# Kernel tuning notes

Hardware: AMD Instinct MI355X
Metric: run time of the kernel (lower is better)

Reference implementation:

```python
import jax, jax.numpy as jnp
import numpy as np
from jax import lax

B, C_IN, N, C_OUT, K = 16, 128, 2048, 256, 20
EPS = 1e-5


def setup_inputs() -> dict:
    key = jax.random.key(0)
    k1, k2 = jax.random.split(key)
    x = jax.random.normal(k1, (B, C_IN, N), dtype=jnp.float32)
    W = jax.random.normal(k2, (C_OUT, 2 * C_IN), dtype=jnp.float32) * (1.0 / np.sqrt(2 * C_IN))
    gamma = jnp.ones((C_OUT,), dtype=jnp.float32)
    beta = jnp.zeros((C_OUT,), dtype=jnp.float32)
    return {"x": x, "W": W, "gamma": gamma, "beta": beta, "k": K}


def _knn_inds(x, k):
    # squared pairwise distance: (B, N, N); computed with no grad (stop_gradient)
    xs = lax.stop_gradient(x)
    inner = jnp.einsum('bcn,bcm->bnm', xs, xs)
    sq = jnp.sum(xs * xs, axis=1)  # (B, N)
    pd = sq[:, :, None] - 2.0 * inner + sq[:, None, :]
    _, inds = lax.top_k(-pd, k)  # smallest distances -> (B, N, k)
    return inds


def reference(x, W, gamma, beta, k):
    knn = _knn_inds(x, k)                                   # (B, N, k) int
    # gather neighbours: neigh[b,c,n,j] = x[b,c,knn[b,n,j]]
    neigh = jax.vmap(lambda xb, kb: xb[:, kb])(x, knn)      # (B, C, N, k)
    central = jnp.broadcast_to(x[:, :, :, None], neigh.shape)
    edge = jnp.concatenate([central, neigh - central], axis=1)  # (B, 2C, N, k)
    # 1x1 conv (bias-free) as GEMM
    y = jnp.einsum('oc,bcnk->bonk', W, edge)                # (B, C_out, N, k)
    # BatchNorm2d (training-mode batch stats) + affine
    mean = jnp.mean(y, axis=(0, 2, 3), keepdims=True)
    var = jnp.var(y, axis=(0, 2, 3), keepdims=True)
    y = (y - mean) * lax.rsqrt(var + EPS)
    y = y * gamma[None, :, None, None] + beta[None, :, None, None]
    y = jax.nn.relu(y)
    return jnp.max(y, axis=3)                               # (B, C_out, N)
```

## Files before the change

### kernel.cpp

```cpp
#include <hip/hip_runtime.h>

#define B_   16
#define CIN  128
#define NPT  2048
#define COUT 256
#define KNN  20
#define KEEP 16
#define SIFT 32
#define EPS  1e-5f
#define DBIAS 256.0f

#define SQ_OFF   0ull
#define IDX_OFF  131072ull
#define UT_OFF   2752512ull
#define VT_OFF   36306944ull
#define GS_OFF   69861376ull
#define ST_OFF   69865472ull
#define AMAX_OFF 69871616ull
#define AMIN_OFF 103426048ull
#define WS_NEED_FUSED 136980480ull
#define XT_OFF   UT_OFF
#define XHT_OFF  VT_OFF

typedef _Float16 f16x8 __attribute__((ext_vector_type(8)));
typedef float    f32x4 __attribute__((ext_vector_type(4)));
typedef float    f32x2 __attribute__((ext_vector_type(2)));

__global__ __launch_bounds__(256) void prep_kernel(const float* __restrict__ x,
                                                   float* __restrict__ xT,
                                                   _Float16* __restrict__ xhT,
                                                   float* __restrict__ sqh) {
    __shared__ float Ls[128 * 68];
    __shared__ float ps[4 * 64];
    const int id  = blockIdx.x;
    const int xcd = id & 7, qq = id >> 3;
    const int b   = xcd + ((qq >> 5) << 3);
    const int n0  = (qq & 31) * 64;
    const int t = threadIdx.x;
    const float* xb = x + (size_t)b * CIN * NPT;
    #pragma unroll
    for (int e = 0; e < 8; ++e) {
        int f = e * 256 + t;
        int c = f >> 4, n4 = (f & 15) << 2;
        *(float4*)&Ls[c * 68 + n4] = *(const float4*)&xb[(size_t)c * NPT + n0 + n4];
    }
    __syncthreads();
    {
        int nl = t & 63, part = t >> 6;
        float acc = 0.f;
        #pragma unroll
        for (int j = 0; j < 32; ++j) {
            float vh = (float)(_Float16)Ls[(part * 32 + j) * 68 + nl];
            acc += vh * vh;
        }
        ps[part * 64 + nl] = acc;
    }
    #pragma unroll
    for (int e = 0; e < 2; ++e) {
        int u = e * 256 + t;
        int nl = u >> 3, ck = (u & 7) << 4;
        float vv[16];
        #pragma unroll
        for (int j = 0; j < 16; ++j) vv[j] = Ls[(ck + j) * 68 + nl];
        size_t row = (size_t)b * NPT + n0 + nl;
        #pragma unroll
        for (int j = 0; j < 4; ++j) {
            float4 w = {vv[4 * j], vv[4 * j + 1], vv[4 * j + 2], vv[4 * j + 3]};
            *(float4*)&xT[row * CIN + ck + 4 * j] = w;
        }
        f16x8 h0, h1;
        #pragma unroll
        for (int j = 0; j < 8; ++j) { h0[j] = (_Float16)vv[j]; h1[j] = (_Float16)vv[8 + j]; }
        *(f16x8*)&xhT[row * CIN + ck] = h0;
        *(f16x8*)&xhT[row * CIN + ck + 8] = h1;
    }
    __syncthreads();
    if (t < 64) sqh[b * NPT + n0 + t] = ps[t] + ps[64 + t] + ps[128 + t] + ps[192 + t];
}

__global__ void wconv_kernel(const float* __restrict__ W,
                             _Float16* __restrict__ Wu,
                             _Float16* __restrict__ Wv) {
    int gid = blockIdx.x * 256 + threadIdx.x;
    int o = gid >> 7, c = gid & 127;
    float w1 = W[o * 256 + c], w2 = W[o * 256 + 128 + c];
    Wu[gid] = (_Float16)(w1 - w2);
    Wv[gid] = (_Float16)w2;
}

__device__ __forceinline__ void stage_pts(const _Float16* __restrict__ xhb,
                                          _Float16* buf, int base_n, int t) {
    const int l15 = t & 15, ks = t >> 6;
    const int quad = (t >> 4) & 3;
    const int c = ks * 32 + quad * 8;
    #pragma unroll
    for (int e = 0; e < 4; ++e) {
        const int n = base_n + e * 16 + l15;
        const _Float16* src = xhb + (size_t)n * CIN + c;
        _Float16* dst = buf + (size_t)(e * 256 + (t & 192)) * 8;
        __builtin_amdgcn_global_load_lds(
            (const __attribute__((address_space(1))) void*)src,
            (__attribute__((address_space(3))) void*)dst, 16, 0, 0);
    }
}

__device__ __forceinline__ void stage_tile16(const _Float16* __restrict__ srcl,
                                             _Float16* dsthalf) {
    #pragma unroll
    for (int e = 0; e < 4; ++e) {
        __builtin_amdgcn_global_load_lds(
            (const __attribute__((address_space(1))) void*)(srcl + e * 32),
            (__attribute__((address_space(3))) void*)(dsthalf + (size_t)e * 512),
            16, 0, 0);
    }
}

__global__ __launch_bounds__(256, 2) void knn_kernel(const _Float16* __restrict__ xhT,
                                                     const float* __restrict__ sqh,
                                                     int* __restrict__ surv_out) {
    __shared__ char smraw[59392];
    _Float16* bufA = (_Float16*)smraw;
    float*    sqm  = (float*)(smraw + 18432);

    const int id  = blockIdx.x;
    const int xcd = id & 7, qq = id >> 3;
    const int b   = xcd + ((qq >> 5) << 3);
    const int q0  = (qq & 31) * 64;
    const int t  = threadIdx.x;
    const int lane = t & 63, wv = t >> 6;
    const int l15 = lane & 15, quad = lane >> 4;
    const _Float16* xhb = xhT + (size_t)b * NPT * CIN;

    #pragma unroll
    for (int e = 0; e < 8; ++e)
        sqm[e * 256 + t] = sqh[b * NPT + e * 256 + t] + DBIAS;

    stage_pts(xhb, bufA, q0, t);
    __syncthreads();

    f16x8 af[4][4];
    #pragma unroll
    for (int qh = 0; qh < 4; ++qh)
        #pragma unroll
        for (int ks = 0; ks < 4; ++ks)
            af[qh][ks] = *(const f16x8*)(bufA + (size_t)((qh * 4 + ks) * 64 + lane) * 8);
    __syncthreads();

    _Float16* wbuf = (_Float16*)(smraw + 26624 + wv * 8192);
    float*    DtW  = (float*)(smraw + wv * 4608);
    const _Float16* srcl = xhb + (size_t)(wv * 16 + l15) * CIN + quad * 8;

    stage_tile16(srcl, wbuf);

    float bd[KEEP];
    #pragma unroll
    for (int i = 0; i < KEEP; ++i) bd[i] = 3.0e38f;

    #pragma unroll 1
    for (int ss = 0; ss < 32; ++ss) {
        const int mb = ss * 64 + wv * 16;
        asm volatile("s_waitcnt vmcnt(0)" ::: "memory");
        __builtin_amdgcn_sched_barrier(0);
        const _Float16* cur = wbuf + (ss & 1) * 2048;
        f16x8 bf[4];
        #pragma unroll
        for (int ks = 0; ks < 4; ++ks)
            bf[ks] = *(const f16x8*)(cur + ks * 512 + lane * 8);
        float sm_ = sqm[mb + l15];
        asm volatile("s_waitcnt lgkmcnt(0)" ::: "memory");
        __builtin_amdgcn_sched_barrier(0);
        if (ss < 31)
            stage_tile16(srcl + (size_t)(ss + 1) * 64 * CIN,
                         wbuf + ((ss + 1) & 1) * 2048);
        __builtin_amdgcn_sched_barrier(0);
        f32x4 acc[4];
        #pragma unroll
        for (int qh = 0; qh < 4; ++qh) acc[qh] = (f32x4){0.f, 0.f, 0.f, 0.f};
        #pragma unroll
        for (int ks = 0; ks < 4; ++ks)
            #pragma unroll
            for (int qh = 0; qh < 4; ++qh)
                acc[qh] = __builtin_amdgcn_mfma_f32_16x16x32_f16(af[qh][ks], bf[ks], acc[qh], 0, 0, 0);
        const unsigned om = (unsigned)(mb + l15);
        #pragma unroll
        for (int qh = 0; qh < 4; ++qh) {
            #pragma unroll
            for (int rg = 0; rg < 4; ++rg) {
                int q = qh * 16 + quad * 4 + rg;
                float d = sm_ - 2.f * acc[qh][rg];
                DtW[q * 18 + l15] = __uint_as_float((__float_as_uint(d) & 0xFFFFF800u) | om);
            }
        }
        float nk[16];
        {
            const float* myrow = DtW + lane * 18;
            #pragma unroll
            for (int p = 0; p < 8; ++p) {
                f32x2 v = *(const f32x2*)(myrow + 2 * p);
                nk[2 * p] = v[0]; nk[2 * p + 1] = v[1];
            }
        }
        #pragma unroll
        for (int kk = 2; kk <= 16; kk <<= 1) {
            #pragma unroll
            for (int j = kk >> 1; j > 0; j >>= 1) {
                #pragma unroll
                for (int i = 0; i < 16; ++i) {
                    int p = i ^ j;
                    if (p > i) {
                        float a = nk[i], c = nk[p];
                        float lo = fminf(a, c), hi = fmaxf(a, c);
                        if ((i & kk) == 0) { nk[i] = lo; nk[p] = hi; }
                        else               { nk[i] = hi; nk[p] = lo; }
                    }
                }
            }
        }
        #pragma unroll
        for (int i = 0; i < 16; ++i) bd[i] = fminf(bd[i], nk[15 - i]);
        #pragma unroll
        for (int j = 8; j > 0; j >>= 1) {
            #pragma unroll
            for (int i = 0; i < 16; ++i) {
                int p = i ^ j;
                if (p > i) {
                    float a = bd[i], c = bd[p];
                    bd[i] = fminf(a, c);
                    bd[p] = fmaxf(a, c);
                }
            }
        }
    }

    __syncthreads();

    float* Keys = (float*)smraw;
    #pragma unroll
    for (int i = 0; i < KEEP; ++i)
        Keys[lane * 65 + wv * KEEP + i] = bd[i];
    __syncthreads();
    {
        int cnt[KEEP];
        #pragma unroll
        for (int i = 0; i < KEEP; ++i) cnt[i] = 0;
        #pragma unroll 4
        for (int j = 0; j < 64; ++j) {
            float kj = Keys[lane * 65 + j];
            #pragma unroll
            for (int i = 0; i < KEEP; ++i)
                cnt[i] += (kj < bd[i]) ? 1 : 0;
        }
        int* dst = surv_out + ((size_t)b * NPT + q0 + lane) * SIFT;
        #pragma unroll
        for (int i = 0; i < KEEP; ++i)
            if (cnt[i] < SIFT)
                dst[cnt[i]] = (int)(__float_as_uint(bd[i]) & 0x7FFu);
    }
}

__global__ __launch_bounds__(256, 4) void refine_kernel(const float* __restrict__ xT,
                                                        const int* __restrict__ surv,
                                                        int* __restrict__ knn_out) {
    __shared__ float  Qs[16 * 128];
    __shared__ int    sidx[16 * 32];
    __shared__ double ddL[16 * 32];
    const int id  = blockIdx.x;
    const int xcd = id & 7, qq = id >> 3;
    const int b   = xcd + ((qq >> 7) << 3);
    const int q0  = (qq & 127) * 16;
    const int t = threadIdx.x;
    const float* xTb = xT + (size_t)b * NPT * CIN;
    #pragma unroll
    for (int e = 0; e < 2; ++e)
        sidx[e * 256 + t] = surv[((size_t)b * NPT + q0) * SIFT + e * 256 + t];
    #pragma unroll
    for (int e = 0; e < 2; ++e) {
        int f = e * 256 + t;
        int row = f >> 5, c4 = (f & 31) << 2;
        *(float4*)&Qs[row * 128 + c4] = *(const float4*)&xTb[(size_t)(q0 + row) * CIN + c4];
    }
    __syncthreads();
    const int g = t >> 3, j = t & 7;
    #pragma unroll 1
    for (int it = 0; it < 16; ++it) {
        int pair = it * 32 + g;
        int q = pair >> 5, k = pair & 31;
        int m = sidx[q * 32 + k];
        const float* mrow = xTb + (size_t)m * CIN + j * 16;
        const float* qrow = Qs + q * 128 + j * 16;
        float4 a0 = *(const float4*)&mrow[0];
        float4 a1 = *(const float4*)&mrow[4];
        float4 a2 = *(const float4*)&mrow[8];
        float4 a3 = *(const float4*)&mrow[12];
        float4 c0 = *(const float4*)&qrow[0];
        float4 c1 = *(const float4*)&qrow[4];
        float4 c2 = *(const float4*)&qrow[8];
        float4 c3 = *(const float4*)&qrow[12];
        double ss = 0.0, d0;
        d0 = (double)c0.x - (double)a0.x; ss = fma(d0, d0, ss);
        d0 = (double)c0.y - (double)a0.y; ss = fma(d0, d0, ss);
        d0 = (double)c0.z - (double)a0.z; ss = fma(d0, d0, ss);
        d0 = (double)c0.w - (double)a0.w; ss = fma(d0, d0, ss);
        d0 = (double)c1.x - (double)a1.x; ss = fma(d0, d0, ss);
        d0 = (double)c1.y - (double)a1.y; ss = fma(d0, d0, ss);
        d0 = (double)c1.z - (double)a1.z; ss = fma(d0, d0, ss);
        d0 = (double)c1.w - (double)a1.w; ss = fma(d0, d0, ss);
        d0 = (double)c2.x - (double)a2.x; ss = fma(d0, d0, ss);
        d0 = (double)c2.y - (double)a2.y; ss = fma(d0, d0, ss);
        d0 = (double)c2.z - (double)a2.z; ss = fma(d0, d0, ss);
        d0 = (double)c2.w - (double)a2.w; ss = fma(d0, d0, ss);
        d0 = (double)c3.x - (double)a3.x; ss = fma(d0, d0, ss);
        d0 = (double)c3.y - (double)a3.y; ss = fma(d0, d0, ss);
        d0 = (double)c3.z - (double)a3.z; ss = fma(d0, d0, ss);
        d0 = (double)c3.w - (double)a3.w; ss = fma(d0, d0, ss);
        ss += __shfl_xor(ss, 1, 8);
        ss += __shfl_xor(ss, 2, 8);
        ss += __shfl_xor(ss, 4, 8);
        if (j == 0) ddL[q * 32 + k] = ss;
    }
    __syncthreads();
    const int q = t >> 4, kk = (t & 15) << 1;
    int* dst = knn_out + ((size_t)b * NPT + q0 + q) * KNN;
    #pragma unroll
    for (int e = 0; e < 2; ++e) {
        int k = kk + e;
        double mine = ddL[q * 32 + k];
        int c = 0;
        #pragma unroll 4
        for (int jx = 0; jx < SIFT; ++jx)
            c += (ddL[q * 32 + jx] < mine) ? 1 : 0;
        if (c < KNN) dst[c] = sidx[q * 32 + k];
    }
}

__global__ __launch_bounds__(256, 2) void knn_kernel_fb(const _Float16* __restrict__ xhT,
                                                        const float* __restrict__ xT,
                                                        const float* __restrict__ sqh,
                                                        int* __restrict__ knn_out) {
    __shared__ char smraw[59392];
    _Float16* bufA = (_Float16*)smraw;
    float*    sqm  = (float*)(smraw + 18432);

    const int b  = blockIdx.y;
    const int q0 = blockIdx.x * 64;
    const int t  = threadIdx.x;
    const int lane = t & 63, wv = t >> 6;
    const int l15 = lane & 15, quad = lane >> 4;
    const _Float16* xhb = xhT + (size_t)b * NPT * CIN;

    #pragma unroll
    for (int e = 0; e < 8; ++e)
        sqm[e * 256 + t] = sqh[b * NPT + e * 256 + t] + DBIAS;

    stage_pts(xhb, bufA, q0, t);
    __syncthreads();

    f16x8 af[4][4];
    #pragma unroll
    for (int qh = 0; qh < 4; ++qh)
        #pragma unroll
        for (int ks = 0; ks < 4; ++ks)
            af[qh][ks] = *(const f16x8*)(bufA + (size_t)((qh * 4 + ks) * 64 + lane) * 8);
    __syncthreads();

    _Float16* wbuf = (_Float16*)(smraw + 26624 + wv * 8192);
    float*    DtW  = (float*)(smraw + wv * 4608);
    const _Float16* srcl = xhb + (size_t)(wv * 16 + l15) * CIN + quad * 8;
    stage_tile16(srcl, wbuf);

    float bd[KEEP];
    #pragma unroll
    for (int i = 0; i < KEEP; ++i) bd[i] = 3.0e38f;

    #pragma unroll 1
    for (int ss = 0; ss < 32; ++ss) {
        const int mb = ss * 64 + wv * 16;
        asm volatile("s_waitcnt vmcnt(0)" ::: "memory");
        __builtin_amdgcn_sched_barrier(0);
        const _Float16* cur = wbuf + (ss & 1) * 2048;
        f16x8 bf[4];
        #pragma unroll
        for (int ks = 0; ks < 4; ++ks)
            bf[ks] = *(const f16x8*)(cur + ks * 512 + lane * 8);
        float sm_ = sqm[mb + l15];
        asm volatile("s_waitcnt lgkmcnt(0)" ::: "memory");
        __builtin_amdgcn_sched_barrier(0);
        if (ss < 31)
            stage_tile16(srcl + (size_t)(ss + 1) * 64 * CIN,
                         wbuf + ((ss + 1) & 1) * 2048);
        __builtin_amdgcn_sched_barrier(0);
        f32x4 acc[4];
        #pragma unroll
        for (int qh = 0; qh < 4; ++qh) acc[qh] = (f32x4){0.f, 0.f, 0.f, 0.f};
        #pragma unroll
        for (int ks = 0; ks < 4; ++ks)
            #pragma unroll
            for (int qh = 0; qh < 4; ++qh)
                acc[qh] = __builtin_amdgcn_mfma_f32_16x16x32_f16(af[qh][ks], bf[ks], acc[qh], 0, 0, 0);
        const unsigned om = (unsigned)(mb + l15);
        #pragma unroll
        for (int qh = 0; qh < 4; ++qh) {
            #pragma unroll
            for (int rg = 0; rg < 4; ++rg) {
                int q = qh * 16 + quad * 4 + rg;
                float d = sm_ - 2.f * acc[qh][rg];
                DtW[q * 18 + l15] = __uint_as_float((__float_as_uint(d) & 0xFFFFF800u) | om);
            }
        }
        float nk[16];
        {
            const float* myrow = DtW + lane * 18;
            #pragma unroll
            for (int p = 0; p < 8; ++p) {
                f32x2 v = *(const f32x2*)(myrow + 2 * p);
                nk[2 * p] = v[0]; nk[2 * p + 1] = v[1];
            }
        }
        #pragma unroll
        for (int kk = 2; kk <= 16; kk <<= 1) {
            #pragma unroll
            for (int j = kk >> 1; j > 0; j >>= 1) {
                #pragma unroll
                for (int i = 0; i < 16; ++i) {
                    int p = i ^ j;
                    if (p > i) {
                        float a = nk[i], c = nk[p];
                        float lo = fminf(a, c), hi = fmaxf(a, c);
                        if ((i & kk) == 0) { nk[i] = lo; nk[p] = hi; }
                        else               { nk[i] = hi; nk[p] = lo; }
                    }
                }
            }
        }
        #pragma unroll
        for (int i = 0; i < 16; ++i) bd[i] = fminf(bd[i], nk[15 - i]);
        #pragma unroll
        for (int j = 8; j > 0; j >>= 1) {
            #pragma unroll
            for (int i = 0; i < 16; ++i) {
                int p = i ^ j;
                if (p > i) {
                    float a = bd[i], c = bd[p];
                    bd[i] = fminf(a, c);
                    bd[p] = fmaxf(a, c);
                }
            }
        }
    }

    __syncthreads();

    float*  Keys = (float*)smraw;
    int*    Surv = (int*)(smraw + 16640);
    double* ddL  = (double*)(smraw + 25088);
    #pragma unroll
    for (int i = 0; i < KEEP; ++i)
        Keys[lane * 65 + wv * KEEP + i] = bd[i];
    __syncthreads();
    {
        int cnt[KEEP];
        #pragma unroll
        for (int i = 0; i < KEEP; ++i) cnt[i] = 0;
        #pragma unroll 4
        for (int j = 0; j < 64; ++j) {
            float kj = Keys[lane * 65 + j];
            #pragma unroll
            for (int i = 0; i < KEEP; ++i)
                cnt[i] += (kj < bd[i]) ? 1 : 0;
        }
        __syncthreads();
        #pragma unroll
        for (int i = 0; i < KEEP; ++i)
            if (cnt[i] < SIFT)
                Surv[lane * 33 + cnt[i]] = (int)(__float_as_uint(bd[i]) & 0x7FFu);
    }
    __syncthreads();

    int ms[8];
    #pragma unroll
    for (int k = 0; k < 8; ++k) ms[k] = Surv[lane * 33 + wv * 8 + k] & 2047;
    double dd8[8];
    #pragma unroll
    for (int k = 0; k < 8; ++k) dd8[k] = 0.0;
    const float* xTb = xT + (size_t)b * NPT * CIN;
    const float* qrow = xTb + (size_t)(q0 + lane) * CIN;
    #pragma unroll 1
    for (int ch = 0; ch < 8; ++ch) {
        double qd[16];
        #pragma unroll
        for (int j = 0; j < 4; ++j) {
            float4 qv = *(const float4*)&qrow[ch * 16 + 4 * j];
            qd[4 * j] = (double)qv.x; qd[4 * j + 1] = (double)qv.y;
            qd[4 * j + 2] = (double)qv.z; qd[4 * j + 3] = (double)qv.w;
        }
        #pragma unroll
        for (int k = 0; k < 8; ++k) {
            const float* mrow = xTb + (size_t)ms[k] * CIN + ch * 16;
            float4 ma = *(const float4*)&mrow[0];
            float4 mb2 = *(const float4*)&mrow[4];
            float4 mc = *(const float4*)&mrow[8];
            float4 md = *(const float4*)&mrow[12];
            double ss = dd8[k], d0;
            d0 = qd[0]  - (double)ma.x;  ss = fma(d0, d0, ss);
            d0 = qd[1]  - (double)ma.y;  ss = fma(d0, d0, ss);
            d0 = qd[2]  - (double)ma.z;  ss = fma(d0, d0, ss);
            d0 = qd[3]  - (double)ma.w;  ss = fma(d0, d0, ss);
            d0 = qd[4]  - (double)mb2.x; ss = fma(d0, d0, ss);
            d0 = qd[5]  - (double)mb2.y; ss = fma(d0, d0, ss);
            d0 = qd[6]  - (double)mb2.z; ss = fma(d0, d0, ss);
            d0 = qd[7]  - (double)mb2.w; ss = fma(d0, d0, ss);
            d0 = qd[8]  - (double)mc.x;  ss = fma(d0, d0, ss);
            d0 = qd[9]  - (double)mc.y;  ss = fma(d0, d0, ss);
            d0 = qd[10] - (double)mc.z;  ss = fma(d0, d0, ss);
            d0 = qd[11] - (double)mc.w;  ss = fma(d0, d0, ss);
            d0 = qd[12] - (double)md.x;  ss = fma(d0, d0, ss);
            d0 = qd[13] - (double)md.y;  ss = fma(d0, d0, ss);
            d0 = qd[14] - (double)md.z;  ss = fma(d0, d0, ss);
            d0 = qd[15] - (double)md.w;  ss = fma(d0, d0, ss);
            dd8[k] = ss;
        }
    }
    #pragma unroll
    for (int k = 0; k < 8; ++k) ddL[lane * 33 + wv * 8 + k] = dd8[k];
    __syncthreads();
    int* dst = knn_out + ((size_t)b * NPT + q0 + lane) * KNN;
    #pragma unroll
    for (int k = 0; k < 8; ++k) {
        int c = 0;
        #pragma unroll 4
        for (int j = 0; j < SIFT; ++j)
            c += (ddL[lane * 33 + j] < dd8[k]) ? 1 : 0;
        if (c < KNN) dst[c] = ms[k];
    }
}

__global__ __launch_bounds__(256) void uv_gemm_h(const _Float16* __restrict__ xhT,
                                                 const _Float16* __restrict__ Wu,
                                                 const _Float16* __restrict__ Wv,
                                                 float* __restrict__ uT,
                                                 float* __restrict__ vT) {
    __shared__ _Float16 Bx[8192];
    const int id  = blockIdx.x;
    const int xcd = id & 7, qq = id >> 3;
    const int b   = xcd + ((qq >> 5) << 3);
    const int n0  = (qq & 31) * 64;
    const int t = threadIdx.x;
    const int lane = t & 63, w = t >> 6, l15 = lane & 15, quad = lane >> 4;
    stage_pts(xhT + (size_t)b * NPT * CIN, Bx, n0, t);
    __syncthreads();
    f16x8 bf[4];
    #pragma unroll
    for (int ks = 0; ks < 4; ++ks)
        bf[ks] = *(const f16x8*)(Bx + (size_t)((w * 4 + ks) * 64 + lane) * 8);
    const int n = n0 + w * 16 + l15;
    #pragma unroll 1
    for (int ot = 0; ot < 16; ++ot) {
        const _Float16* wu = Wu + (size_t)(ot * 16 + l15) * 128 + quad * 8;
        const _Float16* wv2 = Wv + (size_t)(ot * 16 + l15) * 128 + quad * 8;
        f32x4 au = (f32x4){0.f, 0.f, 0.f, 0.f};
        f32x4 av = (f32x4){0.f, 0.f, 0.f, 0.f};
        #pragma unroll
        for (int ks = 0; ks < 4; ++ks) {
            f16x8 a_u = *(const f16x8*)(wu + ks * 32);
            f16x8 a_v = *(const f16x8*)(wv2 + ks * 32);
            au = __builtin_amdgcn_mfma_f32_16x16x32_f16(a_u, bf[ks], au, 0, 0, 0);
            av = __builtin_amdgcn_mfma_f32_16x16x32_f16(a_v, bf[ks], av, 0, 0, 0);
        }
        size_t base = ((size_t)b * NPT + n) * COUT + ot * 16 + quad * 4;
        *(f32x4*)&uT[base] = au;
        *(f32x4*)&vT[base] = av;
    }
}

__global__ __launch_bounds__(256) void uv_gemm(const float* __restrict__ x,
                                               const float* __restrict__ W,
                                               float* __restrict__ uT,
                                               float* __restrict__ vT) {
    __shared__ float Ax[32 * 64];
    __shared__ float Bu[32 * 68];
    __shared__ float Bv[32 * 68];
    const int b  = blockIdx.z;
    const int n0 = blockIdx.x * 64;
    const int o0 = blockIdx.y * 64;
    const int t  = threadIdx.x;
    const int tx = t & 15, ty = t >> 4;
    const float* xb = x + (size_t)b * CIN * NPT;
    float au[4][4], av_[4][4];
    #pragma unroll
    for (int i = 0; i < 4; ++i)
        #pragma unroll
        for (int j = 0; j < 4; ++j) { au[i][j] = 0.f; av_[i][j] = 0.f; }
    #pragma unroll 1
    for (int kc = 0; kc < 4; ++kc) {
        const int c0 = kc * 32;
        __syncthreads();
        #pragma unroll
        for (int e = 0; e < 2; ++e) {
            int f = e * 256 + t;
            int cz = f >> 4, ni = (f & 15) << 2;
            *(float4*)&Ax[(cz << 6) + ni] = *(const float4*)&xb[(size_t)(c0 + cz) * NPT + n0 + ni];
        }
        #pragma unroll
        for (int e = 0; e < 8; ++e) {
            int ii = e * 256 + t;
            int cz = ii & 31, oj = ii >> 5;
            float w1 = W[(size_t)(o0 + oj) * 256 + c0 + cz];
            float w2 = W[(size_t)(o0 + oj) * 256 + 128 + c0 + cz];
            Bu[cz * 68 + oj] = w1 - w2;
            Bv[cz * 68 + oj] = w2;
        }
        __syncthreads();
        #pragma unroll 8
        for (int cz = 0; cz < 32; ++cz) {
            const float4 a4 = *(const float4*)&Ax[(cz << 6) + (tx << 2)];
            float bu0 = Bu[cz * 68 + (ty << 2) + 0], bv0 = Bv[cz * 68 + (ty << 2) + 0];
            float bu1 = Bu[cz * 68 + (ty << 2) + 1], bv1 = Bv[cz * 68 + (ty << 2) + 1];
            float bu2 = Bu[cz * 68 + (ty << 2) + 2], bv2 = Bv[cz * 68 + (ty << 2) + 2];
            float bu3 = Bu[cz * 68 + (ty << 2) + 3], bv3 = Bv[cz * 68 + (ty << 2) + 3];
            au[0][0] += a4.x * bu0; au[0][1] += a4.x * bu1; au[0][2] += a4.x * bu2; au[0][3] += a4.x * bu3;
            au[1][0] += a4.y * bu0; au[1][1] += a4.y * bu1; au[1][2] += a4.y * bu2; au[1][3] += a4.y * bu3;
            au[2][0] += a4.z * bu0; au[2][1] += a4.z * bu1; au[2][2] += a4.z * bu2; au[2][3] += a4.z * bu3;
            au[3][0] += a4.w * bu0; au[3][1] += a4.w * bu1; au[3][2] += a4.w * bu2; au[3][3] += a4.w * bu3;
            av_[0][0] += a4.x * bv0; av_[0][1] += a4.x * bv1; av_[0][2] += a4.x * bv2; av_[0][3] += a4.x * bv3;
            av_[1][0] += a4.y * bv0; av_[1][1] += a4.y * bv1; av_[1][2] += a4.y * bv2; av_[1][3] += a4.y * bv3;
            av_[2][0] += a4.z * bv0; av_[2][1] += a4.z * bv1; av_[2][2] += a4.z * bv2; av_[2][3] += a4.z * bv3;
            av_[3][0] += a4.w * bv0; av_[3][1] += a4.w * bv1; av_[3][2] += a4.w * bv2; av_[3][3] += a4.w * bv3;
        }
    }
    #pragma unroll
    for (int i = 0; i < 4; ++i) {
        int n = n0 + (tx << 2) + i;
        size_t base = ((size_t)b * NPT + n) * COUT + o0 + (ty << 2);
        float4 u4 = {au[i][0], au[i][1], au[i][2], au[i][3]};
        float4 v4 = {av_[i][0], av_[i][1], av_[i][2], av_[i][3]};
        *(float4*)&uT[base] = u4;
        *(float4*)&vT[base] = v4;
    }
}

__global__ __launch_bounds__(256) void gather_stats(const float* __restrict__ uT,
                                                    const float* __restrict__ vT,
                                                    const int* __restrict__ knn_in,
                                                    double* __restrict__ gsum,
                                                    float* __restrict__ aMax,
                                                    float* __restrict__ aMin) {
    __shared__ int sidx[16 * KNN];
    const int id  = blockIdx.x;
    const int xcd = id & 7, qq = id >> 3;
    const int b   = xcd + ((qq >> 7) << 3);
    const int inner = qq & 127;
    const int n0  = (inner >> 2) * 64 + (inner & 3) * 16;
    const int o   = threadIdx.x;
    for (int e = o; e < 16 * KNN; e += 256)
        sidx[e] = knn_in[((size_t)b * NPT + n0) * KNN + e];
    __syncthreads();
    const float* ub = uT + ((size_t)b * NPT + n0) * COUT + o;
    const float* vb = vT + (size_t)b * NPT * COUT + o;
    float* amx = aMax + ((size_t)b * NPT + n0) * COUT + o;
    float* amn = aMin + ((size_t)b * NPT + n0) * COUT + o;
    double s1 = 0.0, s2 = 0.0;
    #pragma unroll 1
    for (int s = 0; s < 16; ++s) {
        float u = ub[(size_t)s * COUT];
        float vmax = -3e38f, vmin = 3e38f, vsum = 0.f, vsq = 0.f;
        #pragma unroll
        for (int j = 0; j < KNN; ++j) {
            float v = vb[(size_t)sidx[s * KNN + j] * COUT];
            vmax = fmaxf(vmax, v);
            vmin = fminf(vmin, v);
            vsum += v;
            vsq = fmaf(v, v, vsq);
        }
        s1 += 20.0 * (double)u + (double)vsum;
        s2 += 20.0 * (double)u * (double)u + 2.0 * (double)u * (double)vsum + (double)vsq;
        float y1 = u + vmax;
        float y2 = u + vmin;
        __builtin_nontemporal_store(y1, &amx[(size_t)s * COUT]);
        __builtin_nontemporal_store(y2, &amn[(size_t)s * COUT]);
    }
    atomicAdd(&gsum[o], s1);
    atomicAdd(&gsum[COUT + o], s2);
}

__global__ __launch_bounds__(256) void stats_kernel(const float* __restrict__ uT,
                                                    const float* __restrict__ vT,
                                                    const int* __restrict__ knn_in,
                                                    double* __restrict__ gsum) {
    __shared__ int sidx[64 * KNN];
    const int b  = blockIdx.y;
    const int n0 = blockIdx.x * 64;
    const int o  = threadIdx.x;
    for (int e = o; e < 64 * KNN; e += 256)
        sidx[e] = knn_in[((size_t)b * NPT + n0) * KNN + e];
    __syncthreads();
    const float* ub = uT + ((size_t)b * NPT + n0) * COUT + o;
    const float* vb = vT + (size_t)b * NPT * COUT + o;
    double s1 = 0.0, s2 = 0.0;
    #pragma unroll 1
    for (int s = 0; s < 64; ++s) {
        float u = ub[(size_t)s * COUT];
        #pragma unroll
        for (int j = 0; j < KNN; ++j) {
            float y = u + vb[(size_t)sidx[s * KNN + j] * COUT];
            s1 += (double)y;
            s2 = fma((double)y, (double)y, s2);
        }
    }
    atomicAdd(&gsum[o], s1);
    atomicAdd(&gsum[COUT + o], s2);
}

__global__ void finalize_kernel(const double* __restrict__ gsum,
                                const float* __restrict__ gamma,
                                const float* __restrict__ beta,
                                float* __restrict__ st) {
    const int o = threadIdx.x;
    const double M = (double)B_ * NPT * KNN;
    double mean = gsum[o] / M;
    double var  = gsum[COUT + o] / M - mean * mean;
    float inv = 1.0f / sqrtf((float)var + EPS);
    float s = gamma[o] * inv;
    st[o] = s;
    st[COUT + o] = beta[o] - (float)mean * s;
}

__global__ __launch_bounds__(256, 2) void out2_kernel(const float* __restrict__ aMax,
                                                      const float* __restrict__ aMin,
                                                      const float* __restrict__ st,
                                                      float* __restrict__ out) {
    __shared__ float zt[256 * 68];
    const int id  = blockIdx.x;
    const int xcd = id & 7, qq = id >> 3;
    const int b   = xcd + ((qq >> 5) << 3);
    const int n0  = (qq & 31) * 64;
    const int o = threadIdx.x;
    const float s  = st[o];
    const float tt = st[COUT + o];
    const float* amx = aMax + ((size_t)b * NPT + n0) * COUT + o;
    const float* amn = aMin + ((size_t)b * NPT + n0) * COUT + o;
    #pragma unroll 2
    for (int si = 0; si < 64; ++si) {
        float y1 = amx[(size_t)si * COUT];
        float y2 = amn[(size_t)si * COUT];
        float z1 = fmaxf(s * y1 + tt, 0.f);
        float z2 = fmaxf(s * y2 + tt, 0.f);
        zt[o * 68 + si] = fmaxf(z1, z2);
    }
    __syncthreads();
    float* dst = out + ((size_t)b * COUT + o) * NPT + n0;
    #pragma unroll
    for (int i = 0; i < 16; ++i)
        *(float4*)&dst[i * 4] = *(const float4*)&zt[o * 68 + i * 4];
}

__global__ __launch_bounds__(256, 2) void out_kernel(const float* __restrict__ uT,
                                                     const float* __restrict__ vT,
                                                     const int* __restrict__ knn_in,
                                                     const float* __restrict__ st,
                                                     float* __restrict__ out) {
    __shared__ int sidx[64 * KNN];
    __shared__ float zt[256 * 68];
    const int b  = blockIdx.y;
    const int n0 = blockIdx.x * 64;
    const int o  = threadIdx.x;
    for (int e = o; e < 64 * KNN; e += 256)
        sidx[e] = knn_in[((size_t)b * NPT + n0) * KNN + e];
    __syncthreads();
    const float s  = st[o];
    const float tt = st[COUT + o];
    const float* ub = uT + ((size_t)b * NPT + n0) * COUT + o;
    const float* vb = vT + (size_t)b * NPT * COUT + o;
    #pragma unroll 1
    for (int si = 0; si < 64; ++si) {
        float u = ub[(size_t)si * COUT];
        float ymax = -3e38f, ymin = 3e38f;
        #pragma unroll
        for (int j = 0; j < KNN; ++j) {
            float y = u + vb[(size_t)sidx[si * KNN + j] * COUT];
            ymax = fmaxf(ymax, y);
            ymin = fminf(ymin, y);
        }
        float z1 = fmaxf(s * ymax + tt, 0.f);
        float z2 = fmaxf(s * ymin + tt, 0.f);
        zt[o * 68 + si] = fmaxf(z1, z2);
    }
    __syncthreads();
    float* dst = out + ((size_t)b * COUT + o) * NPT + n0;
    #pragma unroll
    for (int i = 0; i < 16; ++i)
        *(float4*)&dst[i * 4] = *(const float4*)&zt[o * 68 + i * 4];
}

extern "C" void kernel_launch(void* const* d_in, const int* in_sizes, int n_in,
                              void* d_out, int out_size, void* d_ws, size_t ws_size,
                              hipStream_t stream) {
    const float* x     = (const float*)d_in[0];
    const float* W     = (const float*)d_in[1];
    const float* gamma = (const float*)d_in[2];
    const float* beta  = (const float*)d_in[3];
    float* out = (float*)d_out;
    char* ws = (char*)d_ws;
    float*     sqh  = (float*)(ws + SQ_OFF);
    int*       idx  = (int*)(ws + IDX_OFF);
    float*     uT   = (float*)(ws + UT_OFF);
    float*     vT   = (float*)(ws + VT_OFF);
    double*    gsum = (double*)(ws + GS_OFF);
    float*     st   = (float*)(ws + ST_OFF);
    float*     aMax = (float*)(ws + AMAX_OFF);
    float*     aMin = (float*)(ws + AMIN_OFF);
    const bool fused = (ws_size >= WS_NEED_FUSED);

    hipMemsetAsync(gsum, 0, 2 * COUT * sizeof(double), stream);
    if (fused) {
        float*    xT  = (float*)(ws + AMAX_OFF);
        _Float16* xhT = (_Float16*)(ws + AMAX_OFF + 16777216ull);
        _Float16* Wu  = (_Float16*)(ws + AMAX_OFF + 25165824ull);
        _Float16* Wv  = (_Float16*)(ws + AMAX_OFF + 25231360ull);
        int*      svG = (int*)(ws + UT_OFF);
        prep_kernel<<<512, 256, 0, stream>>>(x, xT, xhT, sqh);
        wconv_kernel<<<128, 256, 0, stream>>>(W, Wu, Wv);
        knn_kernel<<<512, 256, 0, stream>>>(xhT, sqh, svG);
        refine_kernel<<<2048, 256, 0, stream>>>(xT, svG, idx);
        uv_gemm_h<<<512, 256, 0, stream>>>(xhT, Wu, Wv, uT, vT);
        gather_stats<<<2048, 256, 0, stream>>>(uT, vT, idx, gsum, aMax, aMin);
        finalize_kernel<<<1, 256, 0, stream>>>(gsum, gamma, beta, st);
        out2_kernel<<<512, 256, 0, stream>>>(aMax, aMin, st, out);
    } else {
        float*    xT  = (float*)(ws + XT_OFF);
        _Float16* xhT = (_Float16*)(ws + XHT_OFF);
        prep_kernel<<<512, 256, 0, stream>>>(x, xT, xhT, sqh);
        knn_kernel_fb<<<dim3(32, 16), 256, 0, stream>>>(xhT, xT, sqh, idx);
        uv_gemm<<<dim3(32, 4, 16), 256, 0, stream>>>(x, W, uT, vT);
        stats_kernel<<<dim3(32, 16), 256, 0, stream>>>(uT, vT, idx, gsum);
        finalize_kernel<<<1, 256, 0, stream>>>(gsum, gamma, beta, st);
        out_kernel<<<dim3(32, 16), 256, 0, stream>>>(uT, vT, idx, st, out);
    }
}
```

Baseline: 306.5 us.

## Store u/v and max/min intermediates in fp16 and fold small kernels into neighbours

The u/v GEMM outputs and the per-point max/min activations are now stored as fp16 instead of fp32, halving the memory traffic of the gather_stats and out2 kernels. The weight conversion is merged into prep_kernel, and the BN finalize step is folded into out2_kernel, which drops two launches. The cost is reduced precision in the intermediates, which could shift BN outputs slightly, and every out2 block now recomputes the BN scale and shift from the double sums.

```diff
diff --git a/kernel.cpp b/kernel.cpp
--- a/kernel.cpp
+++ b/kernel.cpp
@@ -23,12 +23,16 @@
 #define XHT_OFF  VT_OFF
 
 typedef _Float16 f16x8 __attribute__((ext_vector_type(8)));
+typedef _Float16 f16x4 __attribute__((ext_vector_type(4)));
 typedef float    f32x4 __attribute__((ext_vector_type(4)));
 typedef float    f32x2 __attribute__((ext_vector_type(2)));
 
 __global__ __launch_bounds__(256) void prep_kernel(const float* __restrict__ x,
+                                                   const float* __restrict__ W,
                                                    float* __restrict__ xT,
                                                    _Float16* __restrict__ xhT,
+                                                   _Float16* __restrict__ Wu,
+                                                   _Float16* __restrict__ Wv,
                                                    float* __restrict__ sqh) {
     __shared__ float Ls[128 * 68];
     __shared__ float ps[4 * 64];
@@ -37,6 +41,13 @@
     const int b   = xcd + ((qq >> 5) << 3);
     const int n0  = (qq & 31) * 64;
     const int t = threadIdx.x;
+    if (Wu != nullptr && id < 128) {
+        int gid = id * 256 + t;
+        int o = gid >> 7, c = gid & 127;
+        float w1 = W[o * 256 + c], w2 = W[o * 256 + 128 + c];
+        Wu[gid] = (_Float16)(w1 - w2);
+        Wv[gid] = (_Float16)w2;
+    }
     const float* xb = x + (size_t)b * CIN * NPT;
     #pragma unroll
     for (int e = 0; e < 8; ++e) {
@@ -76,16 +87,6 @@
     }
     __syncthreads();
     if (t < 64) sqh[b * NPT + n0 + t] = ps[t] + ps[64 + t] + ps[128 + t] + ps[192 + t];
-}
-
-__global__ void wconv_kernel(const float* __restrict__ W,
-                             _Float16* __restrict__ Wu,
-                             _Float16* __restrict__ Wv) {
-    int gid = blockIdx.x * 256 + threadIdx.x;
-    int o = gid >> 7, c = gid & 127;
-    float w1 = W[o * 256 + c], w2 = W[o * 256 + 128 + c];
-    Wu[gid] = (_Float16)(w1 - w2);
-    Wv[gid] = (_Float16)w2;
 }
 
 __device__ __forceinline__ void stage_pts(const _Float16* __restrict__ xhb,
@@ -537,8 +538,8 @@
 __global__ __launch_bounds__(256) void uv_gemm_h(const _Float16* __restrict__ xhT,
                                                  const _Float16* __restrict__ Wu,
                                                  const _Float16* __restrict__ Wv,
-                                                 float* __restrict__ uT,
-                                                 float* __restrict__ vT) {
+                                                 _Float16* __restrict__ uT,
+                                                 _Float16* __restrict__ vT) {
     __shared__ _Float16 Bx[8192];
     const int id  = blockIdx.x;
     const int xcd = id & 7, qq = id >> 3;
@@ -567,8 +568,10 @@
             av = __builtin_amdgcn_mfma_f32_16x16x32_f16(a_v, bf[ks], av, 0, 0, 0);
         }
         size_t base = ((size_t)b * NPT + n) * COUT + ot * 16 + quad * 4;
-        *(f32x4*)&uT[base] = au;
-        *(f32x4*)&vT[base] = av;
+        f16x4 auh = {(_Float16)au[0], (_Float16)au[1], (_Float16)au[2], (_Float16)au[3]};
+        f16x4 avh = {(_Float16)av[0], (_Float16)av[1], (_Float16)av[2], (_Float16)av[3]};
+        *(f16x4*)&uT[base] = auh;
+        *(f16x4*)&vT[base] = avh;
     }
 }
 
@@ -638,12 +641,12 @@
     }
 }
 
-__global__ __launch_bounds__(256) void gather_stats(const float* __restrict__ uT,
-                                                    const float* __restrict__ vT,
+__global__ __launch_bounds__(256) void gather_stats(const _Float16* __restrict__ uT,
+                                                    const _Float16* __restrict__ vT,
                                                     const int* __restrict__ knn_in,
                                                     double* __restrict__ gsum,
-                                                    float* __restrict__ aMax,
-                                                    float* __restrict__ aMin) {
+                                                    _Float16* __restrict__ aMax,
+                                                    _Float16* __restrict__ aMin) {
     __shared__ int sidx[16 * KNN];
     const int id  = blockIdx.x;
     const int xcd = id & 7, qq = id >> 3;
@@ -654,18 +657,18 @@
     for (int e = o; e < 16 * KNN; e += 256)
         sidx[e] = knn_in[((size_t)b * NPT + n0) * KNN + e];
     __syncthreads();
-    const float* ub = uT + ((size_t)b * NPT + n0) * COUT + o;
-    const float* vb = vT + (size_t)b * NPT * COUT + o;
-    float* amx = aMax + ((size_t)b * NPT + n0) * COUT + o;
-    float* amn = aMin + ((size_t)b * NPT + n0) * COUT + o;
+    const _Float16* ub = uT + ((size_t)b * NPT + n0) * COUT + o;
+    const _Float16* vb = vT + (size_t)b * NPT * COUT + o;
+    _Float16* amx = aMax + ((size_t)b * NPT + n0) * COUT + o;
+    _Float16* amn = aMin + ((size_t)b * NPT + n0) * COUT + o;
     double s1 = 0.0, s2 = 0.0;
     #pragma unroll 1
     for (int s = 0; s < 16; ++s) {
-        float u = ub[(size_t)s * COUT];
+        float u = (float)ub[(size_t)s * COUT];
         float vmax = -3e38f, vmin = 3e38f, vsum = 0.f, vsq = 0.f;
         #pragma unroll
         for (int j = 0; j < KNN; ++j) {
-            float v = vb[(size_t)sidx[s * KNN + j] * COUT];
+            float v = (float)vb[(size_t)sidx[s * KNN + j] * COUT];
             vmax = fmaxf(vmax, v);
             vmin = fminf(vmin, v);
             vsum += v;
@@ -673,8 +676,8 @@
         }
         s1 += 20.0 * (double)u + (double)vsum;
         s2 += 20.0 * (double)u * (double)u + 2.0 * (double)u * (double)vsum + (double)vsq;
-        float y1 = u + vmax;
-        float y2 = u + vmin;
+        _Float16 y1 = (_Float16)(u + vmax);
+        _Float16 y2 = (_Float16)(u + vmin);
         __builtin_nontemporal_store(y1, &amx[(size_t)s * COUT]);
         __builtin_nontemporal_store(y2, &amn[(size_t)s * COUT]);
     }
@@ -724,9 +727,11 @@
     st[COUT + o] = beta[o] - (float)mean * s;
 }
 
-__global__ __launch_bounds__(256, 2) void out2_kernel(const float* __restrict__ aMax,
-                                                      const float* __restrict__ aMin,
-                                                      const float* __restrict__ st,
+__global__ __launch_bounds__(256, 2) void out2_kernel(const _Float16* __restrict__ aMax,
+                                                      const _Float16* __restrict__ aMin,
+                                                      const double* __restrict__ gsum,
+                                                      const float* __restrict__ gamma,
+                                                      const float* __restrict__ beta,
                                                       float* __restrict__ out) {
     __shared__ float zt[256 * 68];
     const int id  = blockIdx.x;
@@ -734,14 +739,18 @@
     const int b   = xcd + ((qq >> 5) << 3);
     const int n0  = (qq & 31) * 64;
     const int o = threadIdx.x;
-    const float s  = st[o];
-    const float tt = st[COUT + o];
-    const float* amx = aMax + ((size_t)b * NPT + n0) * COUT + o;
-    const float* amn = aMin + ((size_t)b * NPT + n0) * COUT + o;
+    const double M = (double)B_ * NPT * KNN;
+    double mean = gsum[o] / M;
+    double var  = gsum[COUT + o] / M - mean * mean;
+    float inv = 1.0f / sqrtf((float)var + EPS);
+    const float s  = gamma[o] * inv;
+    const float tt = beta[o] - (float)mean * s;
+    const _Float16* amx = aMax + ((size_t)b * NPT + n0) * COUT + o;
+    const _Float16* amn = aMin + ((size_t)b * NPT + n0) * COUT + o;
     #pragma unroll 2
     for (int si = 0; si < 64; ++si) {
-        float y1 = amx[(size_t)si * COUT];
-        float y2 = amn[(size_t)si * COUT];
+        float y1 = (float)amx[(size_t)si * COUT];
+        float y2 = (float)amn[(size_t)si * COUT];
         float z1 = fmaxf(s * y1 + tt, 0.f);
         float z2 = fmaxf(s * y2 + tt, 0.f);
         zt[o * 68 + si] = fmaxf(z1, z2);
@@ -802,33 +811,33 @@
     char* ws = (char*)d_ws;
     float*     sqh  = (float*)(ws + SQ_OFF);
     int*       idx  = (int*)(ws + IDX_OFF);
-    float*     uT   = (float*)(ws + UT_OFF);
-    float*     vT   = (float*)(ws + VT_OFF);
     double*    gsum = (double*)(ws + GS_OFF);
     float*     st   = (float*)(ws + ST_OFF);
-    float*     aMax = (float*)(ws + AMAX_OFF);
-    float*     aMin = (float*)(ws + AMIN_OFF);
     const bool fused = (ws_size >= WS_NEED_FUSED);
 
     hipMemsetAsync(gsum, 0, 2 * COUT * sizeof(double), stream);
     if (fused) {
-        float*    xT  = (float*)(ws + AMAX_OFF);
-        _Float16* xhT = (_Float16*)(ws + AMAX_OFF + 16777216ull);
-        _Float16* Wu  = (_Float16*)(ws + AMAX_OFF + 25165824ull);
-        _Float16* Wv  = (_Float16*)(ws + AMAX_OFF + 25231360ull);
-        int*      svG = (int*)(ws + UT_OFF);
-        prep_kernel<<<512, 256, 0, stream>>>(x, xT, xhT, sqh);
-        wconv_kernel<<<128, 256, 0, stream>>>(W, Wu, Wv);
+        float*    xT   = (float*)(ws + AMAX_OFF);
+        _Float16* xhT  = (_Float16*)(ws + AMAX_OFF + 16777216ull);
+        _Float16* Wu   = (_Float16*)(ws + AMAX_OFF + 25165824ull);
+        _Float16* Wv   = (_Float16*)(ws + AMAX_OFF + 25231360ull);
+        int*      svG  = (int*)(ws + UT_OFF);
+        _Float16* uTh  = (_Float16*)(ws + UT_OFF);
+        _Float16* vTh  = (_Float16*)(ws + VT_OFF);
+        _Float16* aMxh = (_Float16*)(ws + AMAX_OFF);
+        _Float16* aMnh = (_Float16*)(ws + AMIN_OFF);
+        prep_kernel<<<512, 256, 0, stream>>>(x, W, xT, xhT, Wu, Wv, sqh);
         knn_kernel<<<512, 256, 0, stream>>>(xhT, sqh, svG);
         refine_kernel<<<2048, 256, 0, stream>>>(xT, svG, idx);
-        uv_gemm_h<<<512, 256, 0, stream>>>(xhT, Wu, Wv, uT, vT);
-        gather_stats<<<2048, 256, 0, stream>>>(uT, vT, idx, gsum, aMax, aMin);
-        finalize_kernel<<<1, 256, 0, stream>>>(gsum, gamma, beta, st);
-        out2_kernel<<<512, 256, 0, stream>>>(aMax, aMin, st, out);
+        uv_gemm_h<<<512, 256, 0, stream>>>(xhT, Wu, Wv, uTh, vTh);
+        gather_stats<<<2048, 256, 0, stream>>>(uTh, vTh, idx, gsum, aMxh, aMnh);
+        out2_kernel<<<512, 256, 0, stream>>>(aMxh, aMnh, gsum, gamma, beta, out);
     } else {
         float*    xT  = (float*)(ws + XT_OFF);
         _Float16* xhT = (_Float16*)(ws + XHT_OFF);
-        prep_kernel<<<512, 256, 0, stream>>>(x, xT, xhT, sqh);
+        float*    uT  = (float*)(ws + UT_OFF);
+        float*    vT  = (float*)(ws + VT_OFF);
+        prep_kernel<<<512, 256, 0, stream>>>(x, W, xT, xhT, nullptr, nullptr, sqh);
         knn_kernel_fb<<<dim3(32, 16), 256, 0, stream>>>(xhT, xT, sqh, idx);
         uv_gemm<<<dim3(32, 4, 16), 256, 0, stream>>>(x, W, uT, vT);
         stats_kernel<<<dim3(32, 16), 256, 0, stream>>>(uT, vT, idx, gsum);
```

Result: faster. 299.8 us (-2.2%).
